# Kernel tuning notes

Hardware: AMD Instinct MI355X
Metric: run time of the kernel (lower is better)

Reference implementation:

```python
import jax, jax.numpy as jnp
import numpy as np

N = 20000      # num clique nodes
E = 320000     # num edges
H = 256        # hidden_channels
OUT = 128      # out_channels
T = 3          # num_timesteps
NEG = 0.01     # GAT negative_slope
NA = 60000     # num atoms (unused arg sizing)


def setup_inputs() -> dict:
    key = jax.random.key(0)
    ks = jax.random.split(key, 12)
    s = 1.0 / np.sqrt(H)
    return {
        "x_clique": jax.random.normal(ks[0], (N, H), jnp.float32),
        "W_gat": jax.random.normal(ks[1], (H, H), jnp.float32) * s,
        "att_src": jax.random.normal(ks[2], (H,), jnp.float32) * s,
        "att_dst": jax.random.normal(ks[3], (H,), jnp.float32) * s,
        "gat_bias": jnp.zeros((H,), jnp.float32),
        "W_ih": jax.random.normal(ks[4], (3 * H, H), jnp.float32) * s,
        "W_hh": jax.random.normal(ks[5], (3 * H, H), jnp.float32) * s,
        "b_ih": jnp.zeros((3 * H,), jnp.float32),
        "b_hh": jnp.zeros((3 * H,), jnp.float32),
        "lin_W": jax.random.normal(ks[6], (OUT, H), jnp.float32) * s,
        "lin_b": jnp.zeros((OUT,), jnp.float32),
        "atom2clique_index": jax.random.randint(ks[7], (2, NA), 0, N, jnp.int64),
        "mol_batch": jax.random.randint(ks[8], (NA,), 0, 32, jnp.int64),
        "clique_batch": jax.random.randint(ks[9], (N,), 0, 32, jnp.int64),
        "clique_edge_index": jax.random.randint(ks[10], (2, E), 0, N, jnp.int64),
    }


def _gat_conv(h, W_gat, att_src, att_dst, gat_bias, src, dst):
    # PyG GATConv, heads=1, no self loops. h: [N,H]
    xp = h @ W_gat.T                                   # [N,H]
    a_e = jax.nn.leaky_relu((xp @ att_src)[src] + (xp @ att_dst)[dst], NEG)  # [E]
    # segment softmax over destination nodes
    m = jax.ops.segment_max(a_e, dst, num_segments=N)  # [N] (-inf for empty)
    e = jnp.exp(a_e - m[dst])                          # [E]
    denom = jax.ops.segment_sum(e, dst, num_segments=N)
    coef = e / jnp.maximum(denom[dst], 1e-16)          # [E]
    out = jax.ops.segment_sum(coef[:, None] * xp[src], dst, num_segments=N)
    return out + gat_bias


def _gru_cell(x, h, W_ih, W_hh, b_ih, b_hh):
    gx = x @ W_ih.T + b_ih                             # [N,3H]
    gh = h @ W_hh.T + b_hh                             # [N,3H]
    xr, xz, xn = jnp.split(gx, 3, axis=-1)
    hr, hz, hn = jnp.split(gh, 3, axis=-1)
    r = jax.nn.sigmoid(xr + hr)
    z = jax.nn.sigmoid(xz + hz)
    n = jnp.tanh(xn + r * hn)
    return (1.0 - z) * n + z * h


def reference(x_clique, W_gat, att_src, att_dst, gat_bias, W_ih, W_hh, b_ih, b_hh,
              lin_W, lin_b, atom2clique_index, mol_batch, clique_batch,
              clique_edge_index):
    src = clique_edge_index[0]
    dst = clique_edge_index[1]
    h = x_clique
    for _ in range(T):  # fixed, small timestep count
        m = _gat_conv(h, W_gat, att_src, att_dst, gat_bias, src, dst)
        m = jax.nn.elu(m)  # dropout p=0.0 -> identity
        h = _gru_cell(m, h, W_ih, W_hh, b_ih, b_hh)
    return h @ lin_W.T + lin_b  # [N, OUT]
```

## Files before the change

### kernel.cpp

```cpp
#include <hip/hip_runtime.h>
#include <math.h>

#define NNODES 20000
#define NROWP  20096
#define NEDGES 320000
#define HDIM   256
#define ODIM   128
#define TSTEPS 3
#define KCAT   512

typedef __bf16 bf16x8 __attribute__((ext_vector_type(8)));
typedef __bf16 bf16x4 __attribute__((ext_vector_type(4)));
typedef float  f32x4  __attribute__((ext_vector_type(4)));

#define LOG2E 1.44269504f
__device__ __forceinline__ float fexp2_(float x){ return __builtin_amdgcn_exp2f(x); }
__device__ __forceinline__ float frcp_(float x){ return __builtin_amdgcn_rcpf(x); }
__device__ __forceinline__ float fsig_(float x){ return frcp_(1.f + fexp2_(-LOG2E*x)); }
__device__ __forceinline__ float ftanh_(float x){ float t = fexp2_(2.f*LOG2E*x); return 1.f - 2.f*frcp_(t+1.f); }
__device__ __forceinline__ float felu_(float x){ return (x>0.f)? x : (fexp2_(LOG2E*x)-1.f); }

__device__ __forceinline__ void load_lds16(const void* g, void* l){
  __builtin_amdgcn_global_load_lds((const __attribute__((address_space(1))) void*)g,
                                   (__attribute__((address_space(3))) void*)l, 16, 0, 0);
}

__device__ __forceinline__ bf16x8 lds_frag64(const __bf16* Ls, int rowbase, int lane, int kk){
  int row = rowbase + (lane&15);
  int g = (lane>>4) + (kk<<2);
  int slot = (row<<3) + (g ^ (row&7));
  return *(const bf16x8*)&Ls[slot<<3];
}

template<int NWG>
__device__ __forceinline__ int xcd_swz(int b){
  constexpr int Q = NWG/8, R = NWG%8;
  int x = b & 7, i = b >> 3;
  if (R == 0) return x*Q + i;
  return (x < R) ? (x*(Q+1) + i) : (R*(Q+1) + (x-R)*Q + i);
}

__global__ void setup1_kernel(const int* __restrict__ dst, int* __restrict__ deg,
                              const float* __restrict__ xc, __bf16* __restrict__ Acat,
                              const float* __restrict__ Wih, const float* __restrict__ Whh,
                              const float* __restrict__ Wg, const float* __restrict__ Lw,
                              __bf16* __restrict__ Bf, __bf16* __restrict__ wgb,
                              __bf16* __restrict__ lwb, float* __restrict__ asad){
  int i = blockIdx.x*blockDim.x + threadIdx.x;
  if (i < NEDGES) atomicAdd(&deg[dst[i]], 1);
  if (i < NNODES*64){
    int row = i>>6, c = (i&63)<<2;
    float4 v = *(const float4*)&xc[(size_t)row*HDIM + c];
    bf16x4 o; o[0]=(__bf16)v.x; o[1]=(__bf16)v.y; o[2]=(__bf16)v.z; o[3]=(__bf16)v.w;
    *(bf16x4*)&Acat[(size_t)row*KCAT + 256 + c] = o;
  }
  if (i < 1024*128){
    int row = i>>7, kc = (i&127)<<2;
    int gate = row>>8, c = row&255;
    float4 v = make_float4(0,0,0,0);
    if (gate==0 || gate==1){
      v = (kc<256) ? *(const float4*)&Wih[(size_t)(gate*256+c)*HDIM + kc]
                   : *(const float4*)&Whh[(size_t)(gate*256+c)*HDIM + kc-256];
    } else if (gate==2){
      if (kc<256) v = *(const float4*)&Wih[(size_t)(512+c)*HDIM + kc];
    } else {
      if (kc>=256) v = *(const float4*)&Whh[(size_t)(512+c)*HDIM + kc-256];
    }
    bf16x4 o; o[0]=(__bf16)v.x; o[1]=(__bf16)v.y; o[2]=(__bf16)v.z; o[3]=(__bf16)v.w;
    *(bf16x4*)&Bf[(size_t)row*KCAT + kc] = o;
  } else if (i < 1024*128 + 256*64){
    int j = i - 1024*128;
    float4 v = ((const float4*)Wg)[j];
    bf16x4 o; o[0]=(__bf16)v.x; o[1]=(__bf16)v.y; o[2]=(__bf16)v.z; o[3]=(__bf16)v.w;
    ((bf16x4*)wgb)[j] = o;
  } else if (i < 1024*128 + 256*64 + 128*64){
    int j = i - 1024*128 - 256*64;
    float4 v = ((const float4*)Lw)[j];
    bf16x4 o; o[0]=(__bf16)v.x; o[1]=(__bf16)v.y; o[2]=(__bf16)v.z; o[3]=(__bf16)v.w;
    ((bf16x4*)lwb)[j] = o;
  }
  if (i < 2*NNODES) asad[i] = 0.f;
}

__global__ void scan_kernel(const int* __restrict__ deg, int* __restrict__ rowptr){
  const int PER = 20;
  int tid = threadIdx.x, lane = tid&63, w = tid>>6;
  int base = tid*PER;
  int v[PER]; int s = 0;
  #pragma unroll
  for (int k=0;k<PER;k++){
    v[k] = (base+k < NNODES)? deg[base+k] : 0;
    s += v[k];
  }
  int incl = s;
  #pragma unroll
  for (int off=1; off<64; off<<=1){
    int t = __shfl_up(incl, off);
    if (lane >= off) incl += t;
  }
  __shared__ int wtot[16];
  if (lane==63) wtot[w] = incl;
  __syncthreads();
  if (w==0 && lane<16){
    int x = wtot[lane];
    #pragma unroll
    for (int off=1; off<16; off<<=1){
      int t = __shfl_up(x, off);
      if (lane >= off) x += t;
    }
    wtot[lane] = x;
  }
  __syncthreads();
  int wbase = (w>0)? wtot[w-1] : 0;
  int run = wbase + incl - s;
  #pragma unroll
  for (int k=0;k<PER;k++){
    if (base+k < NNODES) rowptr[base+k] = run;
    run += v[k];
  }
  if (tid==1023) rowptr[NNODES] = wbase + incl;
}

__global__ void scatter_kernel(const int* __restrict__ src, const int* __restrict__ dst,
                               const int* __restrict__ rowptr, int* __restrict__ fill,
                               int* __restrict__ ssrc){
  int e = blockIdx.x*blockDim.x + threadIdx.x;
  if (e < NEDGES){
    int d = dst[e];
    int pos = rowptr[d] + atomicAdd(&fill[d], 1);
    ssrc[pos] = src[e];
  }
}

template<int YC, bool F32OUT, bool ALPHA, int NWG>
__global__ __launch_bounds__(256,4)
void mfma_gemm_sm(const __bf16* __restrict__ A, int lda,
                  const __bf16* __restrict__ B,
                  const float* __restrict__ bias,
                  __bf16* __restrict__ Cb, float* __restrict__ Cf,
                  int ldc, int Mreal,
                  const float* __restrict__ att_s, const float* __restrict__ att_d,
                  float* __restrict__ as_, float* __restrict__ ad_){
  __shared__ __bf16 As[64*64];
  __shared__ __bf16 Bs[128*64];
  int wgid = xcd_swz<NWG>(blockIdx.x);
  int r0 = (wgid/YC)*64, c0 = (wgid%YC)*128;
  int tx = threadIdx.x, lane = tx&63, w = tx>>6;
  int rbase = (w&1)*32, cbase = (w>>1)*64;
  f32x4 acc[2][4] = {};
  for (int k0=0; k0<HDIM; k0+=64){
    #pragma unroll
    for (int q=0;q<2;q++){
      int idx = q*256 + w*64 + lane;
      int row = idx>>3, kg = (idx&7) ^ (row&7);
      load_lds16(A + (size_t)(r0+row)*lda + k0 + (kg<<3),
                 (char*)As + (q*256 + w*64)*16);
    }
    #pragma unroll
    for (int q=0;q<4;q++){
      int idx = q*256 + w*64 + lane;
      int row = idx>>3, kg = (idx&7) ^ (row&7);
      load_lds16(B + (size_t)(c0+row)*HDIM + k0 + (kg<<3),
                 (char*)Bs + (q*256 + w*64)*16);
    }
    __syncthreads();
    #pragma unroll
    for (int kk=0;kk<2;kk++){
      bf16x8 a[2], bb[4];
      #pragma unroll
      for (int i=0;i<2;i++) a[i] = lds_frag64(As, rbase + i*16, lane, kk);
      #pragma unroll
      for (int j=0;j<4;j++) bb[j] = lds_frag64(Bs, cbase + j*16, lane, kk);
      #pragma unroll
      for (int i=0;i<2;i++)
        #pragma unroll
        for (int j=0;j<4;j++)
          acc[i][j] = __builtin_amdgcn_mfma_f32_16x16x32_bf16(a[i], bb[j], acc[i][j], 0,0,0);
    }
    __syncthreads();
  }
  int grb = r0 + rbase, gcb = c0 + cbase;
  #pragma unroll
  for (int i=0;i<2;i++){
    #pragma unroll
    for (int j=0;j<4;j++){
      int gc = gcb + j*16 + (lane&15);
      float bv = F32OUT ? bias[gc] : 0.f;
      #pragma unroll
      for (int r=0;r<4;r++){
        int gr = grb + i*16 + ((lane>>4)<<2) + r;
        if (gr >= Mreal) continue;
        float v = acc[i][j][r] + bv;
        if (F32OUT) Cf[(size_t)gr*ldc + gc] = v;
        else        Cb[(size_t)gr*ldc + gc] = (__bf16)v;
      }
    }
  }
  if (ALPHA){
    float ps[2][4] = {}, pd[2][4] = {};
    #pragma unroll
    for (int j=0;j<4;j++){
      int gc = gcb + j*16 + (lane&15);
      float sv = att_s[gc], dv = att_d[gc];
      #pragma unroll
      for (int i=0;i<2;i++)
        #pragma unroll
        for (int r=0;r<4;r++){
          ps[i][r] += acc[i][j][r]*sv;
          pd[i][r] += acc[i][j][r]*dv;
        }
    }
    #pragma unroll
    for (int m=1;m<16;m<<=1){
      #pragma unroll
      for (int i=0;i<2;i++)
        #pragma unroll
        for (int r=0;r<4;r++){
          ps[i][r] += __shfl_xor(ps[i][r], m);
          pd[i][r] += __shfl_xor(pd[i][r], m);
        }
    }
    if ((lane&15)==0){
      #pragma unroll
      for (int i=0;i<2;i++)
        #pragma unroll
        for (int r=0;r<4;r++){
          int gr = grb + i*16 + ((lane>>4)<<2) + r;
          if (gr < Mreal){
            atomicAdd(&as_[gr], ps[i][r]);
            atomicAdd(&ad_[gr], pd[i][r]);
          }
        }
    }
  }
}

__global__ __launch_bounds__(256,4)
void gat_aggregate_kernel(const __bf16* __restrict__ xpb, const float* __restrict__ as_,
                          const float* __restrict__ ad_, const int* __restrict__ rowptr,
                          const int* __restrict__ ssrc, const float* __restrict__ gat_bias,
                          __bf16* __restrict__ Acat){
  int node = blockIdx.x*4 + (threadIdx.x>>6);
  int lane = threadIdx.x & 63;
  if (node >= NNODES) return;
  int beg = rowptr[node], end = rowptr[node+1];
  int deg = end - beg;
  float adv = ad_[node];
  int half = lane>>5, col = lane&31;

  float acc[8] = {0,0,0,0,0,0,0,0};

  if (deg <= 64){
    float a = -INFINITY; int sreg = 0;
    if (lane < deg){
      sreg = ssrc[beg+lane];
      a = as_[sreg] + adv;
      a = (a>0.f)? a : 0.01f*a;
    }
    float mx = a;
    #pragma unroll
    for (int off=32; off; off>>=1) mx = fmaxf(mx, __shfl_xor(mx,off));
    float e = (lane<deg)? fexp2_(LOG2E*(a-mx)) : 0.f;
    float sm = e;
    #pragma unroll
    for (int off=32; off; off>>=1) sm += __shfl_xor(sm,off);
    float creg = e*frcp_(fmaxf(sm,1e-16f));

    int j = 0;
    for (; j+16<=deg; j+=16){
      float cc[8]; int rr[8]; bf16x8 vv[8];
      #pragma unroll
      for (int k=0;k<8;k++){
        cc[k] = __shfl(creg, j+2*k+half);
        rr[k] = __shfl(sreg, j+2*k+half);
      }
      #pragma unroll
      for (int k=0;k<8;k++) vv[k] = *(const bf16x8*)&xpb[(size_t)rr[k]*HDIM + col*8];
      #pragma unroll
      for (int k=0;k<8;k++)
        #pragma unroll
        for (int t=0;t<8;t++) acc[t] += cc[k]*(float)vv[k][t];
    }
    for (; j+8<=deg; j+=8){
      float cc[4]; int rr[4]; bf16x8 vv[4];
      #pragma unroll
      for (int k=0;k<4;k++){
        cc[k] = __shfl(creg, j+2*k+half);
        rr[k] = __shfl(sreg, j+2*k+half);
      }
      #pragma unroll
      for (int k=0;k<4;k++) vv[k] = *(const bf16x8*)&xpb[(size_t)rr[k]*HDIM + col*8];
      #pragma unroll
      for (int k=0;k<4;k++)
        #pragma unroll
        for (int t=0;t<8;t++) acc[t] += cc[k]*(float)vv[k][t];
    }
    for (; j+4<=deg; j+=4){
      float c0=__shfl(creg,j+half),  c1=__shfl(creg,j+2+half);
      int   r0=__shfl(sreg,j+half),  r1=__shfl(sreg,j+2+half);
      bf16x8 v0 = *(const bf16x8*)&xpb[(size_t)r0*HDIM + col*8];
      bf16x8 v1 = *(const bf16x8*)&xpb[(size_t)r1*HDIM + col*8];
      #pragma unroll
      for (int t=0;t<8;t++) acc[t] += c0*(float)v0[t] + c1*(float)v1[t];
    }
    for (; j<deg; j+=2){
      int jj = j + half;
      float cf = __shfl(creg, jj);
      int   rw = __shfl(sreg, jj);
      if (jj < deg){
        bf16x8 v = *(const bf16x8*)&xpb[(size_t)rw*HDIM + col*8];
        #pragma unroll
        for (int t=0;t<8;t++) acc[t] += cf*(float)v[t];
      }
    }
  } else {
    float mx = -INFINITY;
    for (int e=beg+lane; e<end; e+=64){
      float a = as_[ssrc[e]] + adv;
      a = (a>0.f)? a : 0.01f*a;
      mx = fmaxf(mx, a);
    }
    #pragma unroll
    for (int off=32; off; off>>=1) mx = fmaxf(mx, __shfl_xor(mx,off));
    float sm = 0.f;
    for (int e=beg+lane; e<end; e+=64){
      float a = as_[ssrc[e]] + adv;
      a = (a>0.f)? a : 0.01f*a;
      sm += fexp2_(LOG2E*(a-mx));
    }
    #pragma unroll
    for (int off=32; off; off>>=1) sm += __shfl_xor(sm,off);
    float rsc = frcp_(fmaxf(sm,1e-16f));
    for (int j=0; j<deg; j+=2){
      int jj = j + half;
      if (jj < deg){
        int rw = ssrc[beg+jj];
        float a = as_[rw] + adv;
        a = (a>0.f)? a : 0.01f*a;
        float cf = fexp2_(LOG2E*(a-mx))*rsc;
        bf16x8 v = *(const bf16x8*)&xpb[(size_t)rw*HDIM + col*8];
        #pragma unroll
        for (int t=0;t<8;t++) acc[t] += cf*(float)v[t];
      }
    }
  }

  #pragma unroll
  for (int t=0;t<8;t++) acc[t] += __shfl_down(acc[t], 32);
  if (half==0){
    float4 b0 = *(const float4*)&gat_bias[col*8];
    float4 b1 = *(const float4*)&gat_bias[col*8+4];
    float bb[8] = {b0.x,b0.y,b0.z,b0.w,b1.x,b1.y,b1.z,b1.w};
    bf16x8 ov;
    #pragma unroll
    for (int t=0;t<8;t++) ov[t] = (__bf16)felu_(acc[t]+bb[t]);
    *(bf16x8*)&Acat[(size_t)node*KCAT + col*8] = ov;
  }
}

#define RB128 (NROWP/128)
__global__ __launch_bounds__(256,2)
void gru_mfma_kernel(const __bf16* __restrict__ Acat, __bf16* __restrict__ AcatN,
                     const __bf16* __restrict__ Bf,
                     const float* __restrict__ bih, const float* __restrict__ bhh,
                     float* __restrict__ as_, float* __restrict__ ad_){
  __shared__ __bf16 As[2][128*64];
  __shared__ __bf16 Bs[2][96*64];
  int wgid = xcd_swz<RB128*8>(blockIdx.x);
  int r0 = (wgid>>3)*128, c0 = (wgid&7)*32;
  int tx = threadIdx.x, lane = tx&63, w = tx>>6;
  int rbase = w*32;
  f32x4 acc[4][2][2] = {};

  auto stage = [&](int k0, int s, int tg){
    #pragma unroll
    for (int q=0;q<4;q++){
      int idx = q*256 + w*64 + lane;
      int row = idx>>3, kg = (idx&7) ^ (row&7);
      load_lds16(Acat + (size_t)(r0+row)*KCAT + k0 + (kg<<3),
                 (char*)&As[s][0] + (q*256 + w*64)*16);
    }
    #pragma unroll
    for (int q=0;q<3;q++){
      int idx = q*256 + w*64 + lane;
      int row = idx>>3, kg = (idx&7) ^ (row&7);
      int gsel = row>>5;
      int grow = (gsel==2 ? tg : gsel)*256 + c0 + (row&31);
      load_lds16(Bf + (size_t)grow*KCAT + k0 + (kg<<3),
                 (char*)&Bs[s][0] + (q*256 + w*64)*16);
    }
  };

  stage(0, 0, 2);
  __syncthreads();
  #pragma unroll
  for (int t=0; t<KCAT/64; t++){
    const int cur = t & 1;
    if (t+1 < KCAT/64) stage((t+1)*64, cur^1, (t+1<4)?2:3);
    #pragma unroll
    for (int kk=0;kk<2;kk++){
      bf16x8 a[2], b0[2], b1[2], bt[2];
      #pragma unroll
      for (int i=0;i<2;i++) a[i] = lds_frag64(&As[cur][0], rbase + i*16, lane, kk);
      #pragma unroll
      for (int j=0;j<2;j++){
        b0[j] = lds_frag64(&Bs[cur][0], 0  + j*16, lane, kk);
        b1[j] = lds_frag64(&Bs[cur][0], 32 + j*16, lane, kk);
        bt[j] = lds_frag64(&Bs[cur][0], 64 + j*16, lane, kk);
      }
      #pragma unroll
      for (int i=0;i<2;i++)
        #pragma unroll
        for (int j=0;j<2;j++){
          acc[0][i][j] = __builtin_amdgcn_mfma_f32_16x16x32_bf16(a[i], b0[j], acc[0][i][j], 0,0,0);
          acc[1][i][j] = __builtin_amdgcn_mfma_f32_16x16x32_bf16(a[i], b1[j], acc[1][i][j], 0,0,0);
          if (t < 4)
            acc[2][i][j] = __builtin_amdgcn_mfma_f32_16x16x32_bf16(a[i], bt[j], acc[2][i][j], 0,0,0);
          else
            acc[3][i][j] = __builtin_amdgcn_mfma_f32_16x16x32_bf16(a[i], bt[j], acc[3][i][j], 0,0,0);
        }
    }
    __syncthreads();
  }
  int grb = r0 + rbase;
  #pragma unroll
  for (int i=0;i<2;i++){
    #pragma unroll
    for (int j=0;j<2;j++){
      int gc = c0 + j*16 + (lane&15);
      float br_ = bih[gc]     + bhh[gc];
      float bz_ = bih[256+gc] + bhh[256+gc];
      float bnx = bih[512+gc];
      float bnh = bhh[512+gc];
      #pragma unroll
      for (int r=0;r<4;r++){
        int gr = grb + i*16 + ((lane>>4)<<2) + r;
        if (gr >= NNODES) continue;
        float hold = (float)Acat[(size_t)gr*KCAT + 256 + gc];
        float rr = fsig_(acc[0][i][j][r] + br_);
        float zz = fsig_(acc[1][i][j][r] + bz_);
        float nn = ftanh_(acc[2][i][j][r] + bnx + rr*(acc[3][i][j][r] + bnh));
        AcatN[(size_t)gr*KCAT + 256 + gc] = (__bf16)((1.f-zz)*nn + zz*hold);
      }
    }
  }
  if ((wgid&7)==0 && (lane&15)==0){
    #pragma unroll
    for (int i=0;i<2;i++)
      #pragma unroll
      for (int r=0;r<4;r++){
        int gr = grb + i*16 + ((lane>>4)<<2) + r;
        if (gr < NNODES){ as_[gr] = 0.f; ad_[gr] = 0.f; }
      }
  }
}

extern "C" void kernel_launch(void* const* d_in, const int* in_sizes, int n_in,
                              void* d_out, int out_size, void* d_ws, size_t ws_size,
                              hipStream_t stream) {
  const float* x_clique = (const float*)d_in[0];
  const float* W_gat    = (const float*)d_in[1];
  const float* att_src  = (const float*)d_in[2];
  const float* att_dst  = (const float*)d_in[3];
  const float* gat_bias = (const float*)d_in[4];
  const float* W_ih     = (const float*)d_in[5];
  const float* W_hh     = (const float*)d_in[6];
  const float* b_ih     = (const float*)d_in[7];
  const float* b_hh     = (const float*)d_in[8];
  const float* lin_W    = (const float*)d_in[9];
  const float* lin_b    = (const float*)d_in[10];
  const int*   eidx     = (const int*)d_in[14];
  float* out = (float*)d_out;

  const int* src = eidx;
  const int* dst = eidx + NEDGES;

  const size_t ACAT = (size_t)NROWP*KCAT;
  __bf16* AcA  = (__bf16*)d_ws;
  __bf16* AcB  = AcA + ACAT;
  __bf16* xpb  = AcB + ACAT;
  __bf16* Bf   = xpb + (size_t)NROWP*HDIM;
  __bf16* wgb  = Bf  + (size_t)1024*KCAT;
  __bf16* lwb  = wgb + (size_t)HDIM*HDIM;
  float* as_   = (float*)(lwb + (size_t)ODIM*HDIM);
  float* ad_   = as_ + NNODES;
  int* deg     = (int*)(ad_ + NNODES);
  int* fill    = deg + NNODES;
  int* rowptr  = fill + NNODES;
  int* ssrc    = rowptr + (NNODES+1);

  hipMemsetAsync(deg, 0, 2*NNODES*sizeof(int), stream);
  setup1_kernel<<<NNODES*64/256, 256, 0, stream>>>(
      dst, deg, x_clique, AcA, W_ih, W_hh, W_gat, lin_W, Bf, wgb, lwb, as_);
  scan_kernel<<<1, 1024, 0, stream>>>(deg, rowptr);
  scatter_kernel<<<(NEDGES+255)/256, 256, 0, stream>>>(src, dst, rowptr, fill, ssrc);

  const int RB64 = NROWP/64;
  __bf16* Ac = AcA;
  __bf16* An = AcB;
  for (int t=0; t<TSTEPS; t++){
    mfma_gemm_sm<2,false,true,(NROWP/64)*2><<<RB64*2, 256, 0, stream>>>(
        Ac + 256, KCAT, wgb, nullptr, xpb, nullptr, HDIM, NNODES,
        att_src, att_dst, as_, ad_);
    gat_aggregate_kernel<<<(NNODES+3)/4, 256, 0, stream>>>(xpb, as_, ad_, rowptr, ssrc, gat_bias, Ac);
    gru_mfma_kernel<<<RB128*8, 256, 0, stream>>>(Ac, An, Bf, b_ih, b_hh, as_, ad_);
    __bf16* tmp = Ac; Ac = An; An = tmp;
  }
  mfma_gemm_sm<1,true,false,NROWP/64><<<RB64, 256, 0, stream>>>(
      Ac + 256, KCAT, lwb, lin_b, nullptr, out, ODIM, NNODES,
      nullptr, nullptr, nullptr, nullptr);
}
```

Baseline: 354.6 us.

## Double-buffer GEMM LDS stages with explicit vmcnt waits and raw barriers

Gives the projection GEMM a two-stage LDS buffer and prefetches two K-tiles ahead. In the fused GRU GEMM it issues the next tile's loads earlier. Full __syncthreads are replaced by s_waitcnt vmcnt(N) plus s_barrier, so each iteration waits only for the older stage's global-to-LDS loads and the next loads can overlap MFMA work. The cost is doubled LDS in the projection GEMM (occupancy hint lowered from 4 to 3) and correctness that depends on hand-counted vmcnt values.

```diff
diff --git a/kernel.cpp b/kernel.cpp
--- a/kernel.cpp
+++ b/kernel.cpp
@@ -39,6 +39,9 @@
   if (R == 0) return x*Q + i;
   return (x < R) ? (x*(Q+1) + i) : (R*(Q+1) + (x-R)*Q + i);
 }
+
+#define WAIT_VM(n) asm volatile("s_waitcnt vmcnt(" #n ")" ::: "memory")
+#define WAIT_LGKM0 asm volatile("s_waitcnt lgkmcnt(0)" ::: "memory")
 
 __global__ void setup1_kernel(const int* __restrict__ dst, int* __restrict__ deg,
                               const float* __restrict__ xc, __bf16* __restrict__ Acat,
@@ -133,7 +136,7 @@
 }
 
 template<int YC, bool F32OUT, bool ALPHA, int NWG>
-__global__ __launch_bounds__(256,4)
+__global__ __launch_bounds__(256,3)
 void mfma_gemm_sm(const __bf16* __restrict__ A, int lda,
                   const __bf16* __restrict__ B,
                   const float* __restrict__ bias,
@@ -141,43 +144,54 @@
                   int ldc, int Mreal,
                   const float* __restrict__ att_s, const float* __restrict__ att_d,
                   float* __restrict__ as_, float* __restrict__ ad_){
-  __shared__ __bf16 As[64*64];
-  __shared__ __bf16 Bs[128*64];
+  __shared__ __bf16 As[2][64*64];
+  __shared__ __bf16 Bs[2][128*64];
   int wgid = xcd_swz<NWG>(blockIdx.x);
   int r0 = (wgid/YC)*64, c0 = (wgid%YC)*128;
   int tx = threadIdx.x, lane = tx&63, w = tx>>6;
   int rbase = (w&1)*32, cbase = (w>>1)*64;
   f32x4 acc[2][4] = {};
-  for (int k0=0; k0<HDIM; k0+=64){
+
+  auto stage = [&](int k0, int s){
     #pragma unroll
     for (int q=0;q<2;q++){
       int idx = q*256 + w*64 + lane;
       int row = idx>>3, kg = (idx&7) ^ (row&7);
       load_lds16(A + (size_t)(r0+row)*lda + k0 + (kg<<3),
-                 (char*)As + (q*256 + w*64)*16);
+                 (char*)&As[s][0] + (q*256 + w*64)*16);
     }
     #pragma unroll
     for (int q=0;q<4;q++){
       int idx = q*256 + w*64 + lane;
       int row = idx>>3, kg = (idx&7) ^ (row&7);
       load_lds16(B + (size_t)(c0+row)*HDIM + k0 + (kg<<3),
-                 (char*)Bs + (q*256 + w*64)*16);
-    }
-    __syncthreads();
+                 (char*)&Bs[s][0] + (q*256 + w*64)*16);
+    }
+  };
+
+  stage(0, 0);
+  stage(64, 1);
+  #pragma unroll
+  for (int t=0; t<HDIM/64; t++){
+    const int cur = t & 1;
+    if (t == HDIM/64-1) { WAIT_VM(0); } else { WAIT_VM(6); }
+    __builtin_amdgcn_s_barrier();
     #pragma unroll
     for (int kk=0;kk<2;kk++){
       bf16x8 a[2], bb[4];
       #pragma unroll
-      for (int i=0;i<2;i++) a[i] = lds_frag64(As, rbase + i*16, lane, kk);
-      #pragma unroll
-      for (int j=0;j<4;j++) bb[j] = lds_frag64(Bs, cbase + j*16, lane, kk);
+      for (int i=0;i<2;i++) a[i] = lds_frag64(&As[cur][0], rbase + i*16, lane, kk);
+      #pragma unroll
+      for (int j=0;j<4;j++) bb[j] = lds_frag64(&Bs[cur][0], cbase + j*16, lane, kk);
       #pragma unroll
       for (int i=0;i<2;i++)
         #pragma unroll
         for (int j=0;j<4;j++)
           acc[i][j] = __builtin_amdgcn_mfma_f32_16x16x32_bf16(a[i], bb[j], acc[i][j], 0,0,0);
     }
-    __syncthreads();
+    WAIT_LGKM0;
+    __builtin_amdgcn_s_barrier();
+    if (t+2 < HDIM/64) stage((t+2)*64, cur);
   }
   int grb = r0 + rbase, gcb = c0 + cbase;
   #pragma unroll
@@ -392,11 +406,12 @@
   };
 
   stage(0, 0, 2);
-  __syncthreads();
+  stage(64, 1, 2);
   #pragma unroll
   for (int t=0; t<KCAT/64; t++){
     const int cur = t & 1;
-    if (t+1 < KCAT/64) stage((t+1)*64, cur^1, (t+1<4)?2:3);
+    if (t == KCAT/64-1) { WAIT_VM(0); } else { WAIT_VM(7); }
+    __builtin_amdgcn_s_barrier();
     #pragma unroll
     for (int kk=0;kk<2;kk++){
       bf16x8 a[2], b0[2], b1[2], bt[2];
@@ -420,7 +435,9 @@
             acc[3][i][j] = __builtin_amdgcn_mfma_f32_16x16x32_bf16(a[i], bt[j], acc[3][i][j], 0,0,0);
         }
     }
-    __syncthreads();
+    WAIT_LGKM0;
+    __builtin_amdgcn_s_barrier();
+    if (t+2 < KCAT/64) stage((t+2)*64, cur, (t+2<4)?2:3);
   }
   int grb = r0 + rbase;
   #pragma unroll
```

Measured after the change: 353.4 us. About the same (-0.3%).
